# Optimization experiments

Measured on AMD Instinct MI355X. Metric: run time of the kernel, lower is better.

## Reference

```python
import jax, jax.numpy as jnp
import numpy as np

DIM = 8
EPS = 1e-6
TRIL = DIM * (DIM + 1) // 2  # 36


def _build_L(params):
    # params: [N, TRIL] -> lower-triangular L: [N, DIM, DIM] with diag clamped >= 1e-4
    rows, cols = jnp.tril_indices(DIM)
    L = jnp.zeros((params.shape[0], DIM, DIM), params.dtype)
    L = L.at[:, rows, cols].set(params)
    idx = jnp.arange(DIM)
    d = jnp.clip(L[:, idx, idx], 0.0001)
    return L.at[:, idx, idx].set(d)


def _compute_density(L):
    # L: [N, DIM, DIM] -> PSD trace-1 density matrices [N, DIM, DIM]
    I = jnp.eye(DIM, dtype=L.dtype)
    rho = jnp.einsum('nij,nkj->nik', L, L) + EPS * I
    w = jnp.linalg.eigvalsh(rho)                      # [N, DIM]
    corr = jnp.maximum(-w.min(axis=-1), 0.0) + 1e-6   # shift to PSD
    rho = rho + corr[:, None, None] * I
    tr = jnp.trace(rho, axis1=1, axis2=2)
    return rho / (tr[:, None, None] + EPS)


def _matrix_sqrt(x):
    U, S, Vh = jnp.linalg.svd(x, full_matrices=False)
    sqrt_S = jnp.sqrt(S + EPS)
    return (U * sqrt_S[..., None, :]) @ Vh


def _quantum_fidelity(rho, sigma):
    sqrt_rho = _matrix_sqrt(rho)
    product = sqrt_rho @ sigma @ sqrt_rho
    S = jnp.linalg.svd(product, compute_uv=False)
    f = jnp.sum(jnp.sqrt(S + EPS), axis=-1)
    return jnp.clip(f, 0.0, 1.0)


def setup_inputs() -> dict:
    key = jax.random.key(0)
    k1, k2, k3 = jax.random.split(key, 3)
    B, S, V = 16384, 10, 100000
    contexts = jax.random.randint(k1, (B, S), 0, V)
    targets = jax.random.randint(k2, (B,), 0, V)
    # embedding table, init roughly like the torch module (uniform + diag ramp)
    emb_weight = jax.random.uniform(k3, (V, TRIL), jnp.float32, -0.1, 0.1)
    diag_idx = np.array([i * (i + 1) // 2 + i for i in range(DIM)])
    diag_vals = jnp.linspace(0.1, 1.0, DIM, dtype=jnp.float32)
    emb_weight = emb_weight.at[:, diag_idx].set(jnp.broadcast_to(diag_vals, (V, DIM)))
    return {"contexts": contexts, "targets": targets, "emb_weight": emb_weight}


def reference(contexts, targets, emb_weight):
    B, S = contexts.shape
    # context density matrices
    ctx_params = jnp.take(emb_weight, contexts.reshape(-1), axis=0)   # [B*S, TRIL]
    rho_ctx = _compute_density(_build_L(ctx_params)).reshape(B, S, DIM, DIM)
    mask = (contexts != 0).astype(rho_ctx.dtype)[:, :, None, None]
    context_rho = (rho_ctx * mask).sum(axis=1) / mask.sum(axis=1)     # [B, DIM, DIM]
    # target density matrices
    tgt_params = jnp.take(emb_weight, targets, axis=0)                # [B, TRIL]
    rho_tgt = _compute_density(_build_L(tgt_params))                  # [B, DIM, DIM]
    f = _quantum_fidelity(context_rho, rho_tgt)                       # [B]
    return -jnp.log(jnp.clip(f, 1e-8))
```

## Files before the change

### kernel.cpp

```cpp
#include <hip/hip_runtime.h>
#include <math.h>

#define NB   16384
#define SEQ  10
#define DIM  8
#define TRIL 36

__device__ __forceinline__ constexpr int tri(int r, int c) { return r * (r + 1) / 2 + c; }

template <int CTRL>
__device__ __forceinline__ float fperm(float v) {
    return __int_as_float(__builtin_amdgcn_mov_dpp(__float_as_int(v), CTRL, 0xf, 0xf, true));
}
template <int CTRL>
__device__ __forceinline__ double dperm(double v) {
    long long u = __double_as_longlong(v);
    int lo = (int)(u & 0xffffffffLL);
    int hi = (int)(u >> 32);
    lo = __builtin_amdgcn_mov_dpp(lo, CTRL, 0xf, 0xf, true);
    hi = __builtin_amdgcn_mov_dpp(hi, CTRL, 0xf, 0xf, true);
    return __longlong_as_double(((long long)hi << 32) | (long long)(unsigned)lo);
}

__device__ __forceinline__ double fast_rsqrt(double x) {
    double r = __builtin_amdgcn_rsq(x);
    r = r * (1.5 - 0.5 * x * r * r);
    r = r * (1.5 - 0.5 * x * r * r);
    return r;
}
__device__ __forceinline__ double fast_rcp(double x) {
    double r = __builtin_amdgcn_rcp(x);
    r = r * (2.0 - x * r);
    r = r * (2.0 - x * r);
    return r;
}
__device__ __forceinline__ double fast_sqrt(double x) { return x * fast_rsqrt(x); }

template <bool ACCUM>
__device__ __forceinline__ void add_density(const float* __restrict__ p, double (&dst)[TRIL]) {
    float Lf[TRIL];
    const float4* p4 = (const float4*)p;
    #pragma unroll
    for (int i = 0; i < 9; ++i) {
        float4 v = p4[i];
        Lf[4*i+0] = v.x; Lf[4*i+1] = v.y; Lf[4*i+2] = v.z; Lf[4*i+3] = v.w;
    }
    #pragma unroll
    for (int d = 0; d < DIM; ++d) Lf[tri(d, d)] = fmaxf(Lf[tri(d, d)], 1.0e-4f);

    double tr = 1.6e-5;
    #pragma unroll
    for (int i = 0; i < TRIL; ++i) { double v = (double)Lf[i]; tr += v * v; }
    double inv = fast_rcp(tr + 1.0e-6);

    #pragma unroll
    for (int i = 0; i < DIM; ++i) {
        #pragma unroll
        for (int j = 0; j <= i; ++j) {
            double sum = (i == j) ? 2.0e-6 : 0.0;
            #pragma unroll
            for (int k = 0; k <= j; ++k) sum += (double)Lf[tri(i, k)] * (double)Lf[tri(j, k)];
            if (ACCUM) dst[tri(i, j)] += sum * inv;
            else       dst[tri(i, j)]  = sum * inv;
        }
    }
}

__device__ __forceinline__ void chol36(double (&M)[TRIL]) {
    #pragma unroll
    for (int j = 0; j < DIM; ++j) {
        double d = M[tri(j, j)];
        #pragma unroll
        for (int k = 0; k < j; ++k) d -= M[tri(j, k)] * M[tri(j, k)];
        d = fmax(d, 1.0e-30);
        double invd = fast_rsqrt(d);
        M[tri(j, j)] = d * invd;
        #pragma unroll
        for (int i = j + 1; i < DIM; ++i) {
            double v = M[tri(i, j)];
            #pragma unroll
            for (int k = 0; k < j; ++k) v -= M[tri(i, k)] * M[tri(j, k)];
            M[tri(i, j)] = v * invd;
        }
    }
}

__global__ void __launch_bounds__(64)
qcbow_kernel(const int* __restrict__ contexts,
             const int* __restrict__ targets,
             const float* __restrict__ emb,
             float* __restrict__ out)
{
    const int tid = blockIdx.x * 64 + threadIdx.x;
    const int b = tid >> 2;
    const int g = threadIdx.x & 3;

    double A[TRIL];
    #pragma unroll
    for (int i = 0; i < TRIL; ++i) A[i] = 0.0;
    float cntf = 0.0f;
    for (int s = g; s < SEQ; s += 4) {
        int tok = contexts[b * SEQ + s];
        if (tok != 0) {
            add_density<true>(emb + (size_t)tok * TRIL, A);
            cntf += 1.0f;
        }
    }

    double W[TRIL];
    add_density<false>(emb + (size_t)targets[b] * TRIL, W);

    #pragma unroll
    for (int i = 0; i < TRIL; ++i) A[i] += dperm<0xB1>(A[i]);
    cntf += fperm<0xB1>(cntf);
    #pragma unroll
    for (int i = 0; i < TRIL; ++i) A[i] += dperm<0x4E>(A[i]);
    cntf += fperm<0x4E>(cntf);

    chol36(W);

    double invc = fast_rcp((double)cntf);
    #pragma unroll
    for (int i = 0; i < TRIL; ++i) A[i] *= invc;
    #pragma unroll
    for (int d = 0; d < DIM; ++d) A[tri(d, d)] += 1.0e-6;
    chol36(A);

    double wa[DIM], wb[DIM];
#define PICKW(JA, JB)                                                              \
    {                                                                              \
        _Pragma("unroll")                                                          \
        for (int k = 0; k < DIM; ++k) wa[k] = (k >= (JA)) ? W[tri(k, (JA))] : 0.0; \
        _Pragma("unroll")                                                          \
        for (int k = 0; k < DIM; ++k) wb[k] = (k >= (JB)) ? W[tri(k, (JB))] : 0.0; \
    }
    switch (g) {
        case 0: PICKW(0, 1); break;
        case 1: PICKW(2, 3); break;
        case 2: PICKW(4, 5); break;
        default: PICKW(6, 7); break;
    }
#undef PICKW

    float a[DIM], bb[DIM];
    #pragma unroll
    for (int i = 0; i < DIM; ++i) {
        double sa = 0.0, sb = 0.0;
        #pragma unroll
        for (int k = i; k < DIM; ++k) {
            double lk = A[tri(k, i)];
            sa += lk * wa[k];
            sb += lk * wb[k];
        }
        a[i] = (float)sa; bb[i] = (float)sb;
    }

    for (int sweep = 0; sweep < 8; ++sweep) {
        bool conv = true;
        #pragma unroll
        for (int r = 0; r < 7; ++r) {
            float x = 0.0f, y = 0.0f, z = 0.0f;
            #pragma unroll
            for (int k = 0; k < DIM; ++k) {
                x = fmaf(a[k], a[k], x);
                y = fmaf(bb[k], bb[k], y);
                z = fmaf(a[k], bb[k], z);
            }
            float z2 = z * z;
            float d  = x - y;
            if (z2 > 1.0e-12f * x * y && z2 > 1.0e-12f * d * d) conv = false;
            if (z2 > 1.0e-16f * x * y) {
                float tau = -d * (0.5f * __builtin_amdgcn_rcpf(z));
                float t = __builtin_amdgcn_rcpf(fabsf(tau) + sqrtf(fmaf(tau, tau, 1.0f)));
                t = (tau >= 0.0f) ? t : -t;
                float c = __builtin_amdgcn_rsqf(fmaf(t, t, 1.0f));
                float s = t * c;
                #pragma unroll
                for (int k = 0; k < DIM; ++k) {
                    float na = c * a[k] - s * bb[k];
                    float nb = s * a[k] + c * bb[k];
                    a[k] = na; bb[k] = nb;
                }
            }
            #pragma unroll
            for (int k = 0; k < DIM; ++k) {
                float olda = a[k];
                float sa = (g == 0) ? bb[k] : a[k];
                float ta = fperm<0x93>(sa);
                float tb = fperm<0x39>(bb[k]);
                a[k]  = (g == 0) ? olda : ta;
                bb[k] = (g == 3) ? olda : tb;
            }
        }
        if (sweep >= 2 && __all(conv)) break;
    }

    double xn = 0.0, yn = 0.0;
    #pragma unroll
    for (int k = 0; k < DIM; ++k) {
        xn += (double)a[k] * (double)a[k];
        yn += (double)bb[k] * (double)bb[k];
    }
    double fp = fast_sqrt(xn + 1.0e-6) + fast_sqrt(yn + 1.0e-6);
    fp += dperm<0xB1>(fp);
    fp += dperm<0x4E>(fp);
    if (g == 0) {
        double f = fmin(fp, 1.0);
        f = fmax(f, 1.0e-8);
        out[b] = (float)(-log(f));
    }
}

extern "C" void kernel_launch(void* const* d_in, const int* in_sizes, int n_in,
                              void* d_out, int out_size, void* d_ws, size_t ws_size,
                              hipStream_t stream) {
    const int*   contexts = (const int*)d_in[0];
    const int*   targets  = (const int*)d_in[1];
    const float* emb      = (const float*)d_in[2];
    float*       out      = (float*)d_out;

    qcbow_kernel<<<dim3(NB * 4 / 64), dim3(64), 0, stream>>>(contexts, targets, emb, out);
}
```

Measured before the change: 85.39 us.

## Split context and target Cholesky across lane pairs and balance token loads

Each of the four lanes per sample now loads a fixed set of token indices up front. The lanes split the 10 context tokens plus the target evenly, so no lane does a third context density while the others idle. The two Cholesky factorizations, which previously ran redundantly in every lane, now run once per lane: low lanes factor the context matrix and high lanes factor the target matrix. The needed factor columns and the context factor are then exchanged through DPP lane swaps. This trades serial Cholesky and density work for extra register shuffles, select logic and register pressure.

```diff
diff --git a/kernel.cpp b/kernel.cpp
--- a/kernel.cpp
+++ b/kernel.cpp
@@ -94,21 +94,27 @@
     const int tid = blockIdx.x * 64 + threadIdx.x;
     const int b = tid >> 2;
     const int g = threadIdx.x & 3;
+    const bool isLo = (g < 2);
+
+    const int t1 = contexts[b * SEQ + g];
+    const int t2 = contexts[b * SEQ + g + 4];
+    const int* p3 = isLo ? (contexts + b * SEQ + 8 + g) : (targets + b);
+    const int t3 = *p3;
 
     double A[TRIL];
     #pragma unroll
     for (int i = 0; i < TRIL; ++i) A[i] = 0.0;
     float cntf = 0.0f;
-    for (int s = g; s < SEQ; s += 4) {
-        int tok = contexts[b * SEQ + s];
-        if (tok != 0) {
-            add_density<true>(emb + (size_t)tok * TRIL, A);
-            cntf += 1.0f;
-        }
-    }
+    if (t1 != 0) { add_density<true>(emb + (size_t)t1 * TRIL, A); cntf += 1.0f; }
+    if (t2 != 0) { add_density<true>(emb + (size_t)t2 * TRIL, A); cntf += 1.0f; }
 
     double W[TRIL];
-    add_density<false>(emb + (size_t)targets[b] * TRIL, W);
+    add_density<false>(emb + (size_t)t3 * TRIL, W);
+    if (isLo && t3 != 0) {
+        cntf += 1.0f;
+        #pragma unroll
+        for (int i = 0; i < TRIL; ++i) A[i] += W[i];
+    }
 
     #pragma unroll
     for (int i = 0; i < TRIL; ++i) A[i] += dperm<0xB1>(A[i]);
@@ -117,30 +123,44 @@
     for (int i = 0; i < TRIL; ++i) A[i] += dperm<0x4E>(A[i]);
     cntf += fperm<0x4E>(cntf);
 
-    chol36(W);
-
     double invc = fast_rcp((double)cntf);
     #pragma unroll
     for (int i = 0; i < TRIL; ++i) A[i] *= invc;
     #pragma unroll
     for (int d = 0; d < DIM; ++d) A[tri(d, d)] += 1.0e-6;
+
+    #pragma unroll
+    for (int i = 0; i < TRIL; ++i) A[i] = isLo ? A[i] : W[i];
     chol36(A);
 
-    double wa[DIM], wb[DIM];
-#define PICKW(JA, JB)                                                              \
-    {                                                                              \
-        _Pragma("unroll")                                                          \
-        for (int k = 0; k < DIM; ++k) wa[k] = (k >= (JA)) ? W[tri(k, (JA))] : 0.0; \
-        _Pragma("unroll")                                                          \
-        for (int k = 0; k < DIM; ++k) wb[k] = (k >= (JB)) ? W[tri(k, (JB))] : 0.0; \
+    double wa[DIM], wb[DIM], pa[DIM], pb[DIM];
+    #pragma unroll
+    for (int k = 0; k < DIM; ++k) { wa[k] = 0.0; wb[k] = 0.0; pa[k] = 0.0; pb[k] = 0.0; }
+#define EXTRACT(dst_a, dst_b, JA, JB)                                                  \
+    {                                                                                  \
+        _Pragma("unroll")                                                              \
+        for (int k = 0; k < DIM; ++k) dst_a[k] = (k >= (JA)) ? A[tri(k, (JA))] : 0.0;  \
+        _Pragma("unroll")                                                              \
+        for (int k = 0; k < DIM; ++k) dst_b[k] = (k >= (JB)) ? A[tri(k, (JB))] : 0.0;  \
     }
     switch (g) {
-        case 0: PICKW(0, 1); break;
-        case 1: PICKW(2, 3); break;
-        case 2: PICKW(4, 5); break;
-        default: PICKW(6, 7); break;
-    }
-#undef PICKW
+        case 2: EXTRACT(pa, pb, 0, 1); EXTRACT(wa, wb, 4, 5); break;
+        case 3: EXTRACT(pa, pb, 2, 3); EXTRACT(wa, wb, 6, 7); break;
+        default: break;
+    }
+#undef EXTRACT
+    #pragma unroll
+    for (int k = 0; k < DIM; ++k) {
+        double qa = dperm<0x4E>(pa[k]);
+        double qb = dperm<0x4E>(pb[k]);
+        wa[k] = isLo ? qa : wa[k];
+        wb[k] = isLo ? qb : wb[k];
+    }
+    #pragma unroll
+    for (int i = 0; i < TRIL; ++i) {
+        double t = dperm<0x4E>(A[i]);
+        A[i] = isLo ? A[i] : t;
+    }
 
     float a[DIM], bb[DIM];
     #pragma unroll
```

Measured after the change: 84.83 us. About the same (-0.7%).
